# Kernel optimization log

Measured on AMD Instinct MI355X. Metric: run time of the kernel, lower is better.

Reference implementation:

```python
import jax, jax.numpy as jnp
import numpy as np

NU, NI, NE, NR = 100000, 50000, 200000, 64
D, K, EDGES, L, B = 64, 16, 2000000, 2, 4096
REG = 1e-4


def setup_inputs() -> dict:
    key = jax.random.key(0)
    ks = jax.random.split(key, 18)
    f = lambda k, sh: jax.random.normal(k, sh, dtype=jnp.float32)
    return {
        # embedding tables (init std=0.01 as in the torch module)
        'user_emb_w': f(ks[0], (NU, D)) * 0.01,
        'item_emb_w': f(ks[1], (NI, D)) * 0.01,
        'entity_emb_w': f(ks[2], (NE, D)) * 0.01,
        'relation_emb_w': f(ks[3], (NR, D)) * 0.01,
        # per-layer linear params (stacked over L layers)
        'Wk_w': f(ks[4], (L, D, 2 * D)) * 0.05,
        'Wk_b': f(ks[5], (L, D)) * 0.05,
        'Wa_w': f(ks[6], (L, D, D)) * 0.05,
        'Wa_b': f(ks[7], (L, D)) * 0.05,
        'Wb_w': f(ks[8], (L, D, D)) * 0.05,
        'Wb_b': f(ks[9], (L, D)) * 0.05,
        'edge_norm': jax.random.uniform(ks[10], (EDGES,), dtype=jnp.float32),
        # BPR batch ids
        'user': jax.random.randint(ks[11], (B,), 0, NU, dtype=jnp.int32),
        'pos_item': jax.random.randint(ks[12], (B,), 0, NI, dtype=jnp.int32),
        'neg_item': jax.random.randint(ks[13], (B,), 0, NI, dtype=jnp.int32),
        # interaction graph edge lists
        'edge_u': jax.random.randint(ks[14], (EDGES,), 0, NU, dtype=jnp.int32),
        'edge_i': jax.random.randint(ks[15], (EDGES,), 0, NI, dtype=jnp.int32),
        # KG neighbors: K (relation, entity) pairs per item
        'kg_rel': jax.random.randint(ks[16], (NI, K), 0, NR, dtype=jnp.int32),
        'kg_ent': jax.random.randint(ks[17], (NI, K), 0, NE, dtype=jnp.int32),
    }


def reference(user_emb_w, item_emb_w, entity_emb_w, relation_emb_w,
              Wk_w, Wk_b, Wa_w, Wa_b, Wb_w, Wb_b, edge_norm,
              user, pos_item, neg_item, edge_u, edge_i, kg_rel, kg_ent):
    # KG neighbor gathers (entity/relation tables are constant across layers)
    v = entity_emb_w[kg_ent]        # [NI, K, D]
    r = relation_emb_w[kg_rel]      # [NI, K, D]
    norm = edge_norm[:, None]       # [E, 1]

    u_cur, i_cur = user_emb_w, item_emb_w
    u_sum, i_sum = user_emb_w, item_emb_w
    for l in range(L):
        # --- KG attention (vectorized over all items and neighbors) ---
        hv = v * i_cur[:, None, :]                            # [NI, K, D]
        # concat([hv, hv]) @ Wk.T == hv @ (Wk[:, :D] + Wk[:, D:]).T
        w_eff = Wk_w[l][:, :D] + Wk_w[l][:, D:]               # [D, D]
        proj = jnp.einsum('ikd,od->iko', hv, w_eff) + Wk_b[l]  # [NI, K, D]
        score = jax.nn.leaky_relu(jnp.sum(r * proj, axis=-1), 0.2)  # [NI, K]
        alpha = jax.nn.softmax(score, axis=-1)                # softmax over neighbors
        kg_item = jnp.einsum('ik,ikd->id', alpha, v)          # [NI, D]
        # --- LightGCN propagation (segment scatter-add) ---
        agg_i = jax.ops.segment_sum(norm * u_cur[edge_u], edge_i, num_segments=NI)
        agg_u = jax.ops.segment_sum(norm * i_cur[edge_i], edge_u, num_segments=NU)
        # --- Gated fusion ---
        gate = jax.nn.sigmoid(kg_item @ Wa_w[l].T + Wa_b[l]
                              + agg_i @ Wb_w[l].T + Wb_b[l])
        i_cur = gate * kg_item + (1.0 - gate) * agg_i
        u_cur = agg_u
        u_sum = u_sum + u_cur
        i_sum = i_sum + i_cur

    # --- BPR loss ---
    u_e = u_sum[user]
    pos_e = i_sum[pos_item]
    neg_e = i_sum[neg_item]
    pos_s = jnp.sum(u_e * pos_e, axis=-1)
    neg_s = jnp.sum(u_e * neg_e, axis=-1)
    bpr = -jnp.mean(jnp.log(jax.nn.sigmoid(pos_s - neg_s) + 1e-10))
    l2 = (jnp.sum(u_e ** 2) + jnp.sum(pos_e ** 2) + jnp.sum(neg_e ** 2)) / user.shape[0]
    return bpr + REG * l2
```

## Files before the change

kernel.cpp:

```cpp
#include <hip/hip_runtime.h>
#include <math.h>

constexpr int DD    = 64;
constexpr int KK    = 16;
constexpr int NUs   = 100000;
constexpr int NIs   = 50000;
constexpr int NEs   = 200000;
constexpr int NRs   = 64;
constexpr int NEDGE = 2000000;
constexpr int LAYERS = 2;
constexpr int BB    = 4096;
constexpr float REGf = 1e-4f;

constexpr int SUBB  = 256;
constexpr int NB_I  = (NIs + SUBB - 1) / SUBB;
constexpr int NB_U  = (NUs + SUBB - 1) / SUBB;
constexpr int NBT   = NB_I + NB_U;
constexpr int CH    = 8192;
constexpr int NCHK  = (NEDGE + CH - 1) / CH;

__device__ __forceinline__ float wave_sum_f(float x) {
#pragma unroll
  for (int off = 32; off > 0; off >>= 1) x += __shfl_xor(x, off);
  return x;
}


__global__ __launch_bounds__(256) void bhist_kernel(const int* __restrict__ edge_u,
                                                    const int* __restrict__ edge_i,
                                                    int* __restrict__ gbkt) {
  __shared__ int lcnt[NBT];
  for (int b = threadIdx.x; b < NBT; b += 256) lcnt[b] = 0;
  __syncthreads();
  int base = blockIdx.x * CH;
  for (int k = threadIdx.x; k < CH; k += 256) {
    int e = base + k;
    if (e < NEDGE) {
      atomicAdd(&lcnt[edge_i[e] >> 8], 1);
      atomicAdd(&lcnt[NB_I + (edge_u[e] >> 8)], 1);
    }
  }
  __syncthreads();
  for (int b = threadIdx.x; b < NBT; b += 256) {
    int c = lcnt[b];
    if (c) atomicAdd(&gbkt[b], c);
  }
}

__global__ __launch_bounds__(1024) void bscan_kernel(const int* __restrict__ gbkt,
                                                     int* __restrict__ bktbase,
                                                     int* __restrict__ bktcur,
                                                     int* rp_i, int* rp_u) {
  __shared__ int sv[1024];
  int tid = threadIdx.x;
  int x = (tid < NBT) ? gbkt[tid] : 0;
  bool segU = (tid >= NB_I);
  int v = x;
  sv[tid] = v;
  __syncthreads();
  for (int off = 1; off < 1024; off <<= 1) {
    int y = 0;
    if (tid >= off) {
      int o = tid - off;
      if ((o >= NB_I) == segU) y = sv[o];
    }
    __syncthreads();
    v += y;
    sv[tid] = v;
    __syncthreads();
  }
  if (tid < NBT) {
    int ex = v - x;
    bktbase[tid] = ex;
    bktcur[tid] = ex;
  }
  if (tid == 0) { rp_i[NIs] = NEDGE; rp_u[NUs] = NEDGE; }
}

__global__ __launch_bounds__(256) void bscatter_kernel(const int* __restrict__ edge_u,
                                                       const int* __restrict__ edge_i,
                                                       const float* __restrict__ enorm,
                                                       int* __restrict__ bktcur,
                                                       int2* __restrict__ tmp_i,
                                                       int2* __restrict__ tmp_u) {
  __shared__ int lcnt[NBT];
  __shared__ int lbase[NBT];
  for (int b = threadIdx.x; b < NBT; b += 256) lcnt[b] = 0;
  __syncthreads();
  int base = blockIdx.x * CH;
  for (int k = threadIdx.x; k < CH; k += 256) {
    int e = base + k;
    if (e < NEDGE) {
      atomicAdd(&lcnt[edge_i[e] >> 8], 1);
      atomicAdd(&lcnt[NB_I + (edge_u[e] >> 8)], 1);
    }
  }
  __syncthreads();
  for (int b = threadIdx.x; b < NBT; b += 256) {
    int c = lcnt[b];
    lbase[b] = c ? atomicAdd(&bktcur[b], c) : 0;
    lcnt[b] = 0;
  }
  __syncthreads();
  for (int k = threadIdx.x; k < CH; k += 256) {
    int e = base + k;
    if (e < NEDGE) {
      int it = edge_i[e], u = edge_u[e];
      int wb = __float_as_int(enorm[e]);
      int bi = it >> 8;
      int p = lbase[bi] + atomicAdd(&lcnt[bi], 1);
      tmp_i[p] = make_int2(((it & 255) << 20) | u, wb);
      int bu = NB_I + (u >> 8);
      int q = lbase[bu] + atomicAdd(&lcnt[bu], 1);
      tmp_u[q] = make_int2(((u & 255) << 20) | it, wb);
    }
  }
}

__global__ __launch_bounds__(256) void bsort_kernel(const int* __restrict__ gbkt,
                                                    const int* __restrict__ bktbase,
                                                    const int2* __restrict__ tmp_i,
                                                    const int2* __restrict__ tmp_u,
                                                    int2* __restrict__ pair_i,
                                                    int2* __restrict__ pair_u,
                                                    int* __restrict__ rp_i,
                                                    int* __restrict__ rp_u) {
  int b = blockIdx.x;
  bool isI = (b < NB_I);
  const int2* tmp = isI ? tmp_i : tmp_u;
  int2* po = isI ? pair_i : pair_u;
  int* rp = isI ? rp_i : rp_u;
  int ndst = isI ? NIs : NUs;
  int localb = isI ? b : b - NB_I;
  int start = bktbase[b];
  int size = gbkt[b];
  __shared__ int dcnt[256];
  __shared__ int dpos[256];
  __shared__ int wt[4];
  int tid = threadIdx.x;
  dcnt[tid] = 0;
  __syncthreads();
  for (int k = tid; k < size; k += 256) atomicAdd(&dcnt[tmp[start + k].x >> 20], 1);
  __syncthreads();
  int c = dcnt[tid];
  int lane = tid & 63, wid = tid >> 6;
  int v = c;
#pragma unroll
  for (int off = 1; off < 64; off <<= 1) {
    int y = __shfl_up(v, off);
    if (lane >= off) v += y;
  }
  if (lane == 63) wt[wid] = v;
  __syncthreads();
  int woff = 0;
#pragma unroll
  for (int w = 0; w < 4; ++w)
    if (w < wid) woff += wt[w];
  int excl = woff + v - c;
  dpos[tid] = excl;
  int idx = localb * 256 + tid;
  if (idx < ndst) rp[idx] = start + excl;
  dcnt[tid] = 0;
  __syncthreads();
  for (int k = tid; k < size; k += 256) {
    int2 pw = tmp[start + k];
    int sub = pw.x >> 20;
    int j = dpos[sub] + atomicAdd(&dcnt[sub], 1);
    po[start + j] = make_int2(pw.x & 0xFFFFF, pw.y);
  }
}

__global__ __launch_bounds__(64) void rt_kernel(const float* __restrict__ RE,
                                                const float* __restrict__ Wkw,
                                                const float* __restrict__ Wkb,
                                                float* Rt, float* cvec) {
  int l = blockIdx.x >> 6;
  int n = blockIdx.x & 63;
  int d = threadIdx.x;
  const float* W  = Wkw + (size_t)l * DD * 2 * DD;
  const float* re = RE + n * DD;
  float acc = 0.f;
  for (int o = 0; o < DD; ++o) {
    float w = W[o * 2 * DD + d] + W[o * 2 * DD + DD + d];
    acc += re[o] * w;
  }
  Rt[(l * NRs + n) * DD + d] = acc;
  float p = re[d] * Wkb[l * DD + d];
  p = wave_sum_f(p);
  if (d == 0) cvec[l * NRs + n] = p;
}

__global__ __launch_bounds__(256) void attn_kernel(const float* __restrict__ EE,
                                                   const float* __restrict__ Rt_l,
                                                   const float* __restrict__ c_l,
                                                   const int* __restrict__ kg_ent,
                                                   const int* __restrict__ kg_rel,
                                                   const float* __restrict__ i_cur,
                                                   float* __restrict__ kg_item) {
  int tid = threadIdx.x;
  int l16 = tid & 15;
  int gbase = ((tid & 63) >> 4) << 4;
  int gid = blockIdx.x * 16 + (tid >> 4);
  int ngrp = gridDim.x * 16;
  for (int i = gid; i < NIs; i += ngrp) {
    float4 ic = reinterpret_cast<const float4*>(i_cur + ((size_t)i << 6))[l16];
    int ent = kg_ent[i * KK + l16];
    int rel = kg_rel[i * KK + l16];
    float4 vk[KK];
#pragma unroll
    for (int k = 0; k < KK; ++k) {
      int e = __shfl(ent, gbase + k);
      vk[k] = reinterpret_cast<const float4*>(EE + ((size_t)e << 6))[l16];
    }
    float sc[KK];
#pragma unroll
    for (int k = 0; k < KK; ++k) {
      int rl = __shfl(rel, gbase + k);
      float4 rt = reinterpret_cast<const float4*>(Rt_l + ((size_t)rl << 6))[l16];
      float p = vk[k].x * ic.x * rt.x + vk[k].y * ic.y * rt.y
              + vk[k].z * ic.z * rt.z + vk[k].w * ic.w * rt.w;
      p += __shfl_xor(p, 1); p += __shfl_xor(p, 2);
      p += __shfl_xor(p, 4); p += __shfl_xor(p, 8);
      float s = p + c_l[rl];
      sc[k] = (s >= 0.f) ? s : 0.2f * s;
    }
    float m = sc[0];
#pragma unroll
    for (int k = 1; k < KK; ++k) m = fmaxf(m, sc[k]);
    float ssum = 0.f;
#pragma unroll
    for (int k = 0; k < KK; ++k) { sc[k] = __expf(sc[k] - m); ssum += sc[k]; }
    float inv = 1.f / ssum;
    float4 o = make_float4(0.f, 0.f, 0.f, 0.f);
#pragma unroll
    for (int k = 0; k < KK; ++k) {
      float a = sc[k] * inv;
      o.x += a * vk[k].x; o.y += a * vk[k].y;
      o.z += a * vk[k].z; o.w += a * vk[k].w;
    }
    reinterpret_cast<float4*>(kg_item + ((size_t)i << 6))[l16] = o;
  }
}

__global__ __launch_bounds__(256) void agg2_kernel(
    const int* __restrict__ rp_i, const int2* __restrict__ pair_i,
    const float* __restrict__ embU, float* __restrict__ aggi,
    const int* __restrict__ rp_u, const int2* __restrict__ pair_u,
    const float* __restrict__ embI, float* __restrict__ unext,
    float* __restrict__ usum, const float* __restrict__ usum_init) {
  int tid = threadIdx.x;
  int l16 = tid & 15;
  int gbase = ((tid & 63) >> 4) << 4;
  int gid = blockIdx.x * 16 + (tid >> 4);
  int ngrp = gridDim.x * 16;
  const int total = NIs + NUs;
  for (int row = gid; row < total; row += ngrp) {
    bool isU = row >= NIs;
    int r = isU ? (row - NIs) : row;
    const int*  rp = isU ? rp_u   : rp_i;
    const int2* pr = isU ? pair_u : pair_i;
    const float* emb = isU ? embI : embU;
    int s0 = rp[r], s1 = rp[r + 1];
    float4 accA = make_float4(0.f, 0.f, 0.f, 0.f);
    float4 accB = make_float4(0.f, 0.f, 0.f, 0.f);
    for (int base = s0; base < s1; base += 16) {
      int lim = s1 - base;
      int sj = 0; float wj = 0.f;
      if (l16 < lim) {
        int2 pw = pr[base + l16];
        sj = pw.x; wj = __int_as_float(pw.y);
      }
#pragma unroll
      for (int jj = 0; jj < 8; ++jj) {
        int aA = __shfl(sj, gbase + jj);     float qA = __shfl(wj, gbase + jj);
        int aB = __shfl(sj, gbase + 8 + jj); float qB = __shfl(wj, gbase + 8 + jj);
        float4 eA = reinterpret_cast<const float4*>(emb + ((size_t)aA << 6))[l16];
        float4 eB = reinterpret_cast<const float4*>(emb + ((size_t)aB << 6))[l16];
        accA.x += qA * eA.x; accA.y += qA * eA.y; accA.z += qA * eA.z; accA.w += qA * eA.w;
        accB.x += qB * eB.x; accB.y += qB * eB.y; accB.z += qB * eB.z; accB.w += qB * eB.w;
      }
    }
    float4 o;
    o.x = accA.x + accB.x; o.y = accA.y + accB.y;
    o.z = accA.z + accB.z; o.w = accA.w + accB.w;
    if (!isU) {
      reinterpret_cast<float4*>(aggi + ((size_t)r << 6))[l16] = o;
    } else {
      reinterpret_cast<float4*>(unext + ((size_t)r << 6))[l16] = o;
      float4 si;
      if (usum_init) si = reinterpret_cast<const float4*>(usum_init + ((size_t)r << 6))[l16];
      else           si = reinterpret_cast<float4*>(usum + ((size_t)r << 6))[l16];
      float4 s;
      s.x = si.x + o.x; s.y = si.y + o.y; s.z = si.z + o.z; s.w = si.w + o.w;
      reinterpret_cast<float4*>(usum + ((size_t)r << 6))[l16] = s;
    }
  }
}

__global__ __launch_bounds__(256) void gate_kernel(const float* __restrict__ Wa,
                                                   const float* __restrict__ Wab,
                                                   const float* __restrict__ Wb,
                                                   const float* __restrict__ Wbb,
                                                   const float* __restrict__ kg_item,
                                                   const float* __restrict__ agg_i,
                                                   const float* __restrict__ i_sum_init,
                                                   float* __restrict__ i_next,
                                                   float* __restrict__ i_sum) {
  __shared__ float at[DD * 65];
  __shared__ float bt[DD * 65];
  for (int m = threadIdx.x; m < DD * DD; m += blockDim.x) {
    int o = m >> 6, d = m & 63;
    at[d * 65 + o] = Wa[m];
    bt[d * 65 + o] = Wb[m];
  }
  __syncthreads();
  int lane = threadIdx.x & 63, wid = threadIdx.x >> 6;
  int wpg = gridDim.x * (blockDim.x >> 6);
  float wab = Wab[lane], wbb = Wbb[lane];
  for (int i = blockIdx.x * (blockDim.x >> 6) + wid; i < NIs; i += wpg) {
    float kg = kg_item[i * DD + lane];
    float ag = agg_i[i * DD + lane];
    float acca = 0.f, accb = 0.f;
#pragma unroll
    for (int d = 0; d < DD; ++d) {
      float kd = __shfl(kg, d);
      float ad = __shfl(ag, d);
      acca += kd * at[d * 65 + lane];
      accb += ad * bt[d * 65 + lane];
    }
    float g = 1.f / (1.f + __expf(-(acca + wab + accb + wbb)));
    float inew = g * kg + (1.f - g) * ag;
    i_next[i * DD + lane] = inew;
    if (i_sum_init) i_sum[i * DD + lane] = i_sum_init[i * DD + lane] + inew;
    else            i_sum[i * DD + lane] += inew;
  }
}

__global__ __launch_bounds__(256) void loss_kernel(const float* __restrict__ u_sum,
                                                   const float* __restrict__ i_sum,
                                                   const int* __restrict__ user,
                                                   const int* __restrict__ pos,
                                                   const int* __restrict__ neg,
                                                   float* acc) {
  int lane = threadIdx.x & 63, wid = threadIdx.x >> 6;
  int wpg = gridDim.x * (blockDim.x >> 6);
  float lacc = 0.f, l2acc = 0.f;
  for (int b = blockIdx.x * (blockDim.x >> 6) + wid; b < BB; b += wpg) {
    float u = u_sum[user[b] * DD + lane];
    float p = i_sum[pos[b] * DD + lane];
    float n = i_sum[neg[b] * DD + lane];
    float ps = wave_sum_f(u * p);
    float ns = wave_sum_f(u * n);
    float sq = wave_sum_f(u * u + p * p + n * n);
    if (lane == 0) {
      float x = ps - ns;
      float sig = 1.f / (1.f + expf(-x));
      lacc += logf(sig + 1e-10f);
      l2acc += sq;
    }
  }
  if (lane == 0) {
    atomicAdd(&acc[0], lacc);
    atomicAdd(&acc[1], l2acc);
  }
}

__global__ void final_kernel(const float* acc, float* out) {
  out[0] = -acc[0] / (float)BB + REGf * (acc[1] / (float)BB);
}


extern "C" void kernel_launch(void* const* d_in, const int* in_sizes, int n_in,
                              void* d_out, int out_size, void* d_ws, size_t ws_size,
                              hipStream_t stream) {
  const float* UE   = (const float*)d_in[0];
  const float* IE   = (const float*)d_in[1];
  const float* EE   = (const float*)d_in[2];
  const float* RE   = (const float*)d_in[3];
  const float* Wkw  = (const float*)d_in[4];
  const float* Wkb  = (const float*)d_in[5];
  const float* Waw  = (const float*)d_in[6];
  const float* Wab  = (const float*)d_in[7];
  const float* Wbw  = (const float*)d_in[8];
  const float* Wbb  = (const float*)d_in[9];
  const float* enorm = (const float*)d_in[10];
  const int* user   = (const int*)d_in[11];
  const int* pos    = (const int*)d_in[12];
  const int* neg    = (const int*)d_in[13];
  const int* edge_u = (const int*)d_in[14];
  const int* edge_i = (const int*)d_in[15];
  const int* kg_rel = (const int*)d_in[16];
  const int* kg_ent = (const int*)d_in[17];

  size_t off = 0;
  char* base = (char*)d_ws;
  auto take = [&](size_t bytes) -> void* {
    void* p = base + off;
    off += (bytes + 255) & ~(size_t)255;
    return p;
  };
  float* Rt      = (float*)take(LAYERS * NRs * DD * sizeof(float));
  float* cvec    = (float*)take(LAYERS * NRs * sizeof(float));
  float* acc     = (float*)take(8 * sizeof(float));
  int*   gbkt    = (int*)take(NBT * sizeof(int));
  int*   bktbase = (int*)take(NBT * sizeof(int));
  int*   bktcur  = (int*)take(NBT * sizeof(int));
  int*   rp_i    = (int*)take((NIs + 1) * sizeof(int));
  int*   rp_u    = (int*)take((NUs + 1) * sizeof(int));
  int2*  tmp_i   = (int2*)take((size_t)NEDGE * sizeof(int2));
  int2*  tmp_u   = (int2*)take((size_t)NEDGE * sizeof(int2));
  int2*  pair_i  = (int2*)take((size_t)NEDGE * sizeof(int2));
  int2*  pair_u  = (int2*)take((size_t)NEDGE * sizeof(int2));
  float* kg      = (float*)take((size_t)NIs * DD * sizeof(float));
  float* aggi    = (float*)take((size_t)NIs * DD * sizeof(float));
  float* iA      = (float*)take((size_t)NIs * DD * sizeof(float));
  float* iB      = (float*)take((size_t)NIs * DD * sizeof(float));
  float* isum    = (float*)take((size_t)NIs * DD * sizeof(float));
  float* uA      = (float*)take((size_t)NUs * DD * sizeof(float));
  float* uB      = (float*)take((size_t)NUs * DD * sizeof(float));
  float* usum    = (float*)take((size_t)NUs * DD * sizeof(float));
  (void)ws_size; (void)in_sizes; (void)n_in; (void)out_size;

  hipMemsetAsync(gbkt, 0, NBT * sizeof(int), stream);
  hipMemsetAsync(acc, 0, 8 * sizeof(float), stream);

  bhist_kernel<<<NCHK, 256, 0, stream>>>(edge_u, edge_i, gbkt);
  bscan_kernel<<<1, 1024, 0, stream>>>(gbkt, bktbase, bktcur, rp_i, rp_u);
  bscatter_kernel<<<NCHK, 256, 0, stream>>>(edge_u, edge_i, enorm, bktcur, tmp_i, tmp_u);
  bsort_kernel<<<NBT, 256, 0, stream>>>(gbkt, bktbase, tmp_i, tmp_u,
                                        pair_i, pair_u, rp_i, rp_u);
  rt_kernel<<<LAYERS * NRs, 64, 0, stream>>>(RE, Wkw, Wkb, Rt, cvec);

  const float* u_cur = UE;
  const float* i_cur = IE;
  float* unext[2] = {uA, uB};
  float* inext[2] = {iA, iB};
  for (int l = 0; l < LAYERS; ++l) {
    attn_kernel<<<2048, 256, 0, stream>>>(EE, Rt + l * NRs * DD, cvec + l * NRs,
                                          kg_ent, kg_rel, i_cur, kg);
    agg2_kernel<<<2048, 256, 0, stream>>>(rp_i, pair_i, u_cur, aggi,
                                          rp_u, pair_u, i_cur, unext[l],
                                          usum, (l == 0) ? UE : nullptr);
    gate_kernel<<<2048, 256, 0, stream>>>(Waw + (size_t)l * DD * DD, Wab + l * DD,
                                          Wbw + (size_t)l * DD * DD, Wbb + l * DD,
                                          kg, aggi, (l == 0) ? IE : nullptr,
                                          inext[l], isum);
    u_cur = unext[l];
    i_cur = inext[l];
  }

  loss_kernel<<<1024, 256, 0, stream>>>(usum, isum, user, pos, neg, acc);
  final_kernel<<<1, 1, 0, stream>>>(acc, (float*)d_out);
}
```

Baseline: 941.1 us.

## Fuse attention, aggregation and gating into one per-layer kernel; merge small launches

Merges the KG attention, LightGCN aggregation and gated fusion kernels into a single layer kernel. The kg_item and agg_i intermediates now stay in registers instead of going through global memory. The rt computation is folded into the scan kernel's extra blocks, the memsets become one prep kernel, and the final kernel is replaced by a last-block-done reduction inside the loss kernel, which also drops from 1024 to 256 blocks. In exchange, item rows and user rows now run different code paths inside one kernel, which can cause imbalance, and every block must load the transposed gate weights into shared memory.

```diff
diff --git a/kernel.cpp b/kernel.cpp
--- a/kernel.cpp
+++ b/kernel.cpp
@@ -25,6 +25,12 @@
   return x;
 }
 
+__global__ __launch_bounds__(256) void prep_kernel(int* gbkt, float* acc, int* done) {
+  for (int b = threadIdx.x; b < NBT; b += 256) gbkt[b] = 0;
+  if (threadIdx.x < 8) acc[threadIdx.x] = 0.f;
+  if (threadIdx.x == 8) *done = 0;
+}
+
 
 __global__ __launch_bounds__(256) void bhist_kernel(const int* __restrict__ edge_u,
                                                     const int* __restrict__ edge_i,
@@ -47,34 +53,55 @@
   }
 }
 
-__global__ __launch_bounds__(1024) void bscan_kernel(const int* __restrict__ gbkt,
-                                                     int* __restrict__ bktbase,
-                                                     int* __restrict__ bktcur,
-                                                     int* rp_i, int* rp_u) {
-  __shared__ int sv[1024];
-  int tid = threadIdx.x;
-  int x = (tid < NBT) ? gbkt[tid] : 0;
-  bool segU = (tid >= NB_I);
-  int v = x;
-  sv[tid] = v;
-  __syncthreads();
-  for (int off = 1; off < 1024; off <<= 1) {
-    int y = 0;
-    if (tid >= off) {
-      int o = tid - off;
-      if ((o >= NB_I) == segU) y = sv[o];
-    }
-    __syncthreads();
-    v += y;
+__global__ __launch_bounds__(1024) void bscan_rt_kernel(const int* __restrict__ gbkt,
+                                                        int* __restrict__ bktbase,
+                                                        int* __restrict__ bktcur,
+                                                        int* rp_i, int* rp_u,
+                                                        const float* __restrict__ RE,
+                                                        const float* __restrict__ Wkw,
+                                                        const float* __restrict__ Wkb,
+                                                        float* Rt, float* cvec) {
+  if (blockIdx.x == 0) {
+    __shared__ int sv[1024];
+    int tid = threadIdx.x;
+    int x = (tid < NBT) ? gbkt[tid] : 0;
+    bool segU = (tid >= NB_I);
+    int v = x;
     sv[tid] = v;
     __syncthreads();
-  }
-  if (tid < NBT) {
-    int ex = v - x;
-    bktbase[tid] = ex;
-    bktcur[tid] = ex;
-  }
-  if (tid == 0) { rp_i[NIs] = NEDGE; rp_u[NUs] = NEDGE; }
+    for (int off = 1; off < 1024; off <<= 1) {
+      int y = 0;
+      if (tid >= off) {
+        int o = tid - off;
+        if ((o >= NB_I) == segU) y = sv[o];
+      }
+      __syncthreads();
+      v += y;
+      sv[tid] = v;
+      __syncthreads();
+    }
+    if (tid < NBT) {
+      int ex = v - x;
+      bktbase[tid] = ex;
+      bktcur[tid] = ex;
+    }
+    if (tid == 0) { rp_i[NIs] = NEDGE; rp_u[NUs] = NEDGE; }
+  } else {
+    int p = (blockIdx.x - 1) * 16 + (threadIdx.x >> 6);
+    int l = p >> 6, n = p & 63;
+    int d = threadIdx.x & 63;
+    const float* W  = Wkw + (size_t)l * DD * 2 * DD;
+    const float* re = RE + n * DD;
+    float acc = 0.f;
+    for (int o = 0; o < DD; ++o) {
+      float w = W[o * 2 * DD + d] + W[o * 2 * DD + DD + d];
+      acc += re[o] * w;
+    }
+    Rt[(l * NRs + n) * DD + d] = acc;
+    float pr = re[d] * Wkb[l * DD + d];
+    pr = wave_sum_f(pr);
+    if (d == 0) cvec[l * NRs + n] = pr;
+  }
 }
 
 __global__ __launch_bounds__(256) void bscatter_kernel(const int* __restrict__ edge_u,
@@ -170,84 +197,27 @@
   }
 }
 
-__global__ __launch_bounds__(64) void rt_kernel(const float* __restrict__ RE,
-                                                const float* __restrict__ Wkw,
-                                                const float* __restrict__ Wkb,
-                                                float* Rt, float* cvec) {
-  int l = blockIdx.x >> 6;
-  int n = blockIdx.x & 63;
-  int d = threadIdx.x;
-  const float* W  = Wkw + (size_t)l * DD * 2 * DD;
-  const float* re = RE + n * DD;
-  float acc = 0.f;
-  for (int o = 0; o < DD; ++o) {
-    float w = W[o * 2 * DD + d] + W[o * 2 * DD + DD + d];
-    acc += re[o] * w;
-  }
-  Rt[(l * NRs + n) * DD + d] = acc;
-  float p = re[d] * Wkb[l * DD + d];
-  p = wave_sum_f(p);
-  if (d == 0) cvec[l * NRs + n] = p;
-}
-
-__global__ __launch_bounds__(256) void attn_kernel(const float* __restrict__ EE,
-                                                   const float* __restrict__ Rt_l,
-                                                   const float* __restrict__ c_l,
-                                                   const int* __restrict__ kg_ent,
-                                                   const int* __restrict__ kg_rel,
-                                                   const float* __restrict__ i_cur,
-                                                   float* __restrict__ kg_item) {
-  int tid = threadIdx.x;
-  int l16 = tid & 15;
-  int gbase = ((tid & 63) >> 4) << 4;
-  int gid = blockIdx.x * 16 + (tid >> 4);
-  int ngrp = gridDim.x * 16;
-  for (int i = gid; i < NIs; i += ngrp) {
-    float4 ic = reinterpret_cast<const float4*>(i_cur + ((size_t)i << 6))[l16];
-    int ent = kg_ent[i * KK + l16];
-    int rel = kg_rel[i * KK + l16];
-    float4 vk[KK];
-#pragma unroll
-    for (int k = 0; k < KK; ++k) {
-      int e = __shfl(ent, gbase + k);
-      vk[k] = reinterpret_cast<const float4*>(EE + ((size_t)e << 6))[l16];
-    }
-    float sc[KK];
-#pragma unroll
-    for (int k = 0; k < KK; ++k) {
-      int rl = __shfl(rel, gbase + k);
-      float4 rt = reinterpret_cast<const float4*>(Rt_l + ((size_t)rl << 6))[l16];
-      float p = vk[k].x * ic.x * rt.x + vk[k].y * ic.y * rt.y
-              + vk[k].z * ic.z * rt.z + vk[k].w * ic.w * rt.w;
-      p += __shfl_xor(p, 1); p += __shfl_xor(p, 2);
-      p += __shfl_xor(p, 4); p += __shfl_xor(p, 8);
-      float s = p + c_l[rl];
-      sc[k] = (s >= 0.f) ? s : 0.2f * s;
-    }
-    float m = sc[0];
-#pragma unroll
-    for (int k = 1; k < KK; ++k) m = fmaxf(m, sc[k]);
-    float ssum = 0.f;
-#pragma unroll
-    for (int k = 0; k < KK; ++k) { sc[k] = __expf(sc[k] - m); ssum += sc[k]; }
-    float inv = 1.f / ssum;
-    float4 o = make_float4(0.f, 0.f, 0.f, 0.f);
-#pragma unroll
-    for (int k = 0; k < KK; ++k) {
-      float a = sc[k] * inv;
-      o.x += a * vk[k].x; o.y += a * vk[k].y;
-      o.z += a * vk[k].z; o.w += a * vk[k].w;
-    }
-    reinterpret_cast<float4*>(kg_item + ((size_t)i << 6))[l16] = o;
-  }
-}
-
-__global__ __launch_bounds__(256) void agg2_kernel(
+__global__ __launch_bounds__(256) void layer_kernel(
+    const float* __restrict__ EE, const float* __restrict__ Rt_l,
+    const float* __restrict__ c_l,
+    const int* __restrict__ kg_ent, const int* __restrict__ kg_rel,
+    const float* __restrict__ Waw_l, const float* __restrict__ Wab_l,
+    const float* __restrict__ Wbw_l, const float* __restrict__ Wbb_l,
     const int* __restrict__ rp_i, const int2* __restrict__ pair_i,
-    const float* __restrict__ embU, float* __restrict__ aggi,
     const int* __restrict__ rp_u, const int2* __restrict__ pair_u,
-    const float* __restrict__ embI, float* __restrict__ unext,
-    float* __restrict__ usum, const float* __restrict__ usum_init) {
+    const float* __restrict__ u_cur, const float* __restrict__ i_cur,
+    float* __restrict__ i_next, float* __restrict__ i_sum,
+    const float* __restrict__ i_sum_init,
+    float* __restrict__ u_next, float* __restrict__ u_sum,
+    const float* __restrict__ u_sum_init) {
+  __shared__ float at_s[DD * DD];
+  __shared__ float bt_s[DD * DD];
+  for (int m = threadIdx.x; m < DD * DD; m += 256) {
+    int o = m >> 6, d = m & 63;
+    at_s[d * 64 + o] = Waw_l[m];
+    bt_s[d * 64 + o] = Wbw_l[m];
+  }
+  __syncthreads();
   int tid = threadIdx.x;
   int l16 = tid & 15;
   int gbase = ((tid & 63) >> 4) << 4;
@@ -255,84 +225,143 @@
   int ngrp = gridDim.x * 16;
   const int total = NIs + NUs;
   for (int row = gid; row < total; row += ngrp) {
-    bool isU = row >= NIs;
-    int r = isU ? (row - NIs) : row;
-    const int*  rp = isU ? rp_u   : rp_i;
-    const int2* pr = isU ? pair_u : pair_i;
-    const float* emb = isU ? embI : embU;
-    int s0 = rp[r], s1 = rp[r + 1];
-    float4 accA = make_float4(0.f, 0.f, 0.f, 0.f);
-    float4 accB = make_float4(0.f, 0.f, 0.f, 0.f);
-    for (int base = s0; base < s1; base += 16) {
-      int lim = s1 - base;
-      int sj = 0; float wj = 0.f;
-      if (l16 < lim) {
-        int2 pw = pr[base + l16];
-        sj = pw.x; wj = __int_as_float(pw.y);
-      }
-#pragma unroll
-      for (int jj = 0; jj < 8; ++jj) {
-        int aA = __shfl(sj, gbase + jj);     float qA = __shfl(wj, gbase + jj);
-        int aB = __shfl(sj, gbase + 8 + jj); float qB = __shfl(wj, gbase + 8 + jj);
-        float4 eA = reinterpret_cast<const float4*>(emb + ((size_t)aA << 6))[l16];
-        float4 eB = reinterpret_cast<const float4*>(emb + ((size_t)aB << 6))[l16];
-        accA.x += qA * eA.x; accA.y += qA * eA.y; accA.z += qA * eA.z; accA.w += qA * eA.w;
-        accB.x += qB * eB.x; accB.y += qB * eB.y; accB.z += qB * eB.z; accB.w += qB * eB.w;
-      }
-    }
-    float4 o;
-    o.x = accA.x + accB.x; o.y = accA.y + accB.y;
-    o.z = accA.z + accB.z; o.w = accA.w + accB.w;
-    if (!isU) {
-      reinterpret_cast<float4*>(aggi + ((size_t)r << 6))[l16] = o;
+    if (row < NIs) {
+      int i = row;
+      float4 ic = reinterpret_cast<const float4*>(i_cur + ((size_t)i << 6))[l16];
+      int ent = kg_ent[i * KK + l16];
+      int rel = kg_rel[i * KK + l16];
+      float4 vk[KK];
+#pragma unroll
+      for (int k = 0; k < KK; ++k) {
+        int e = __shfl(ent, gbase + k);
+        vk[k] = reinterpret_cast<const float4*>(EE + ((size_t)e << 6))[l16];
+      }
+      float sc[KK];
+#pragma unroll
+      for (int k = 0; k < KK; ++k) {
+        int rl = __shfl(rel, gbase + k);
+        float4 rt = reinterpret_cast<const float4*>(Rt_l + ((size_t)rl << 6))[l16];
+        float p = vk[k].x * ic.x * rt.x + vk[k].y * ic.y * rt.y
+                + vk[k].z * ic.z * rt.z + vk[k].w * ic.w * rt.w;
+        p += __shfl_xor(p, 1); p += __shfl_xor(p, 2);
+        p += __shfl_xor(p, 4); p += __shfl_xor(p, 8);
+        float s = p + c_l[rl];
+        sc[k] = (s >= 0.f) ? s : 0.2f * s;
+      }
+      float mx = sc[0];
+#pragma unroll
+      for (int k = 1; k < KK; ++k) mx = fmaxf(mx, sc[k]);
+      float ssum = 0.f;
+#pragma unroll
+      for (int k = 0; k < KK; ++k) { sc[k] = __expf(sc[k] - mx); ssum += sc[k]; }
+      float inv = 1.f / ssum;
+      float4 kg = make_float4(0.f, 0.f, 0.f, 0.f);
+#pragma unroll
+      for (int k = 0; k < KK; ++k) {
+        float a = sc[k] * inv;
+        kg.x += a * vk[k].x; kg.y += a * vk[k].y;
+        kg.z += a * vk[k].z; kg.w += a * vk[k].w;
+      }
+      int s0 = rp_i[i], s1 = rp_i[i + 1];
+      float4 accA = make_float4(0.f, 0.f, 0.f, 0.f);
+      float4 accB = make_float4(0.f, 0.f, 0.f, 0.f);
+      for (int base = s0; base < s1; base += 16) {
+        int lim = s1 - base;
+        int sj = 0; float wj = 0.f;
+        if (l16 < lim) {
+          int2 pw = pair_i[base + l16];
+          sj = pw.x; wj = __int_as_float(pw.y);
+        }
+#pragma unroll
+        for (int jj = 0; jj < 8; ++jj) {
+          int aA = __shfl(sj, gbase + jj);     float qA = __shfl(wj, gbase + jj);
+          int aB = __shfl(sj, gbase + 8 + jj); float qB = __shfl(wj, gbase + 8 + jj);
+          float4 eA = reinterpret_cast<const float4*>(u_cur + ((size_t)aA << 6))[l16];
+          float4 eB = reinterpret_cast<const float4*>(u_cur + ((size_t)aB << 6))[l16];
+          accA.x += qA * eA.x; accA.y += qA * eA.y; accA.z += qA * eA.z; accA.w += qA * eA.w;
+          accB.x += qB * eB.x; accB.y += qB * eB.y; accB.z += qB * eB.z; accB.w += qB * eB.w;
+        }
+      }
+      float4 ag;
+      ag.x = accA.x + accB.x; ag.y = accA.y + accB.y;
+      ag.z = accA.z + accB.z; ag.w = accA.w + accB.w;
+      float4 acca = make_float4(0.f, 0.f, 0.f, 0.f);
+      float4 accb = make_float4(0.f, 0.f, 0.f, 0.f);
+#pragma unroll
+      for (int r = 0; r < 16; ++r) {
+        float kx = __shfl(kg.x, gbase + r), ky = __shfl(kg.y, gbase + r);
+        float kz = __shfl(kg.z, gbase + r), kw = __shfl(kg.w, gbase + r);
+        float axv = __shfl(ag.x, gbase + r), ayv = __shfl(ag.y, gbase + r);
+        float azv = __shfl(ag.z, gbase + r), awv = __shfl(ag.w, gbase + r);
+        float4 a0 = *reinterpret_cast<const float4*>(&at_s[(4 * r + 0) * 64 + l16 * 4]);
+        float4 a1 = *reinterpret_cast<const float4*>(&at_s[(4 * r + 1) * 64 + l16 * 4]);
+        float4 a2 = *reinterpret_cast<const float4*>(&at_s[(4 * r + 2) * 64 + l16 * 4]);
+        float4 a3 = *reinterpret_cast<const float4*>(&at_s[(4 * r + 3) * 64 + l16 * 4]);
+        acca.x += kx * a0.x + ky * a1.x + kz * a2.x + kw * a3.x;
+        acca.y += kx * a0.y + ky * a1.y + kz * a2.y + kw * a3.y;
+        acca.z += kx * a0.z + ky * a1.z + kz * a2.z + kw * a3.z;
+        acca.w += kx * a0.w + ky * a1.w + kz * a2.w + kw * a3.w;
+        float4 b0 = *reinterpret_cast<const float4*>(&bt_s[(4 * r + 0) * 64 + l16 * 4]);
+        float4 b1 = *reinterpret_cast<const float4*>(&bt_s[(4 * r + 1) * 64 + l16 * 4]);
+        float4 b2 = *reinterpret_cast<const float4*>(&bt_s[(4 * r + 2) * 64 + l16 * 4]);
+        float4 b3 = *reinterpret_cast<const float4*>(&bt_s[(4 * r + 3) * 64 + l16 * 4]);
+        accb.x += axv * b0.x + ayv * b1.x + azv * b2.x + awv * b3.x;
+        accb.y += axv * b0.y + ayv * b1.y + azv * b2.y + awv * b3.y;
+        accb.z += axv * b0.z + ayv * b1.z + azv * b2.z + awv * b3.z;
+        accb.w += axv * b0.w + ayv * b1.w + azv * b2.w + awv * b3.w;
+      }
+      float4 wab = reinterpret_cast<const float4*>(Wab_l)[l16];
+      float4 wbb = reinterpret_cast<const float4*>(Wbb_l)[l16];
+      float4 g, inew;
+      g.x = 1.f / (1.f + __expf(-(acca.x + wab.x + accb.x + wbb.x)));
+      g.y = 1.f / (1.f + __expf(-(acca.y + wab.y + accb.y + wbb.y)));
+      g.z = 1.f / (1.f + __expf(-(acca.z + wab.z + accb.z + wbb.z)));
+      g.w = 1.f / (1.f + __expf(-(acca.w + wab.w + accb.w + wbb.w)));
+      inew.x = g.x * kg.x + (1.f - g.x) * ag.x;
+      inew.y = g.y * kg.y + (1.f - g.y) * ag.y;
+      inew.z = g.z * kg.z + (1.f - g.z) * ag.z;
+      inew.w = g.w * kg.w + (1.f - g.w) * ag.w;
+      reinterpret_cast<float4*>(i_next + ((size_t)i << 6))[l16] = inew;
+      float4 si;
+      if (i_sum_init) si = reinterpret_cast<const float4*>(i_sum_init + ((size_t)i << 6))[l16];
+      else            si = reinterpret_cast<float4*>(i_sum + ((size_t)i << 6))[l16];
+      float4 so;
+      so.x = si.x + inew.x; so.y = si.y + inew.y;
+      so.z = si.z + inew.z; so.w = si.w + inew.w;
+      reinterpret_cast<float4*>(i_sum + ((size_t)i << 6))[l16] = so;
     } else {
-      reinterpret_cast<float4*>(unext + ((size_t)r << 6))[l16] = o;
+      int r = row - NIs;
+      int s0 = rp_u[r], s1 = rp_u[r + 1];
+      float4 accA = make_float4(0.f, 0.f, 0.f, 0.f);
+      float4 accB = make_float4(0.f, 0.f, 0.f, 0.f);
+      for (int base = s0; base < s1; base += 16) {
+        int lim = s1 - base;
+        int sj = 0; float wj = 0.f;
+        if (l16 < lim) {
+          int2 pw = pair_u[base + l16];
+          sj = pw.x; wj = __int_as_float(pw.y);
+        }
+#pragma unroll
+        for (int jj = 0; jj < 8; ++jj) {
+          int aA = __shfl(sj, gbase + jj);     float qA = __shfl(wj, gbase + jj);
+          int aB = __shfl(sj, gbase + 8 + jj); float qB = __shfl(wj, gbase + 8 + jj);
+          float4 eA = reinterpret_cast<const float4*>(i_cur + ((size_t)aA << 6))[l16];
+          float4 eB = reinterpret_cast<const float4*>(i_cur + ((size_t)aB << 6))[l16];
+          accA.x += qA * eA.x; accA.y += qA * eA.y; accA.z += qA * eA.z; accA.w += qA * eA.w;
+          accB.x += qB * eB.x; accB.y += qB * eB.y; accB.z += qB * eB.z; accB.w += qB * eB.w;
+        }
+      }
+      float4 o;
+      o.x = accA.x + accB.x; o.y = accA.y + accB.y;
+      o.z = accA.z + accB.z; o.w = accA.w + accB.w;
+      reinterpret_cast<float4*>(u_next + ((size_t)r << 6))[l16] = o;
       float4 si;
-      if (usum_init) si = reinterpret_cast<const float4*>(usum_init + ((size_t)r << 6))[l16];
-      else           si = reinterpret_cast<float4*>(usum + ((size_t)r << 6))[l16];
+      if (u_sum_init) si = reinterpret_cast<const float4*>(u_sum_init + ((size_t)r << 6))[l16];
+      else            si = reinterpret_cast<float4*>(u_sum + ((size_t)r << 6))[l16];
       float4 s;
       s.x = si.x + o.x; s.y = si.y + o.y; s.z = si.z + o.z; s.w = si.w + o.w;
-      reinterpret_cast<float4*>(usum + ((size_t)r << 6))[l16] = s;
-    }
-  }
-}
-
-__global__ __launch_bounds__(256) void gate_kernel(const float* __restrict__ Wa,
-                                                   const float* __restrict__ Wab,
-                                                   const float* __restrict__ Wb,
-                                                   const float* __restrict__ Wbb,
-                                                   const float* __restrict__ kg_item,
-                                                   const float* __restrict__ agg_i,
-                                                   const float* __restrict__ i_sum_init,
-                                                   float* __restrict__ i_next,
-                                                   float* __restrict__ i_sum) {
-  __shared__ float at[DD * 65];
-  __shared__ float bt[DD * 65];
-  for (int m = threadIdx.x; m < DD * DD; m += blockDim.x) {
-    int o = m >> 6, d = m & 63;
-    at[d * 65 + o] = Wa[m];
-    bt[d * 65 + o] = Wb[m];
-  }
-  __syncthreads();
-  int lane = threadIdx.x & 63, wid = threadIdx.x >> 6;
-  int wpg = gridDim.x * (blockDim.x >> 6);
-  float wab = Wab[lane], wbb = Wbb[lane];
-  for (int i = blockIdx.x * (blockDim.x >> 6) + wid; i < NIs; i += wpg) {
-    float kg = kg_item[i * DD + lane];
-    float ag = agg_i[i * DD + lane];
-    float acca = 0.f, accb = 0.f;
-#pragma unroll
-    for (int d = 0; d < DD; ++d) {
-      float kd = __shfl(kg, d);
-      float ad = __shfl(ag, d);
-      acca += kd * at[d * 65 + lane];
-      accb += ad * bt[d * 65 + lane];
-    }
-    float g = 1.f / (1.f + __expf(-(acca + wab + accb + wbb)));
-    float inew = g * kg + (1.f - g) * ag;
-    i_next[i * DD + lane] = inew;
-    if (i_sum_init) i_sum[i * DD + lane] = i_sum_init[i * DD + lane] + inew;
-    else            i_sum[i * DD + lane] += inew;
+      reinterpret_cast<float4*>(u_sum + ((size_t)r << 6))[l16] = s;
+    }
   }
 }
 
@@ -341,7 +370,7 @@
                                                    const int* __restrict__ user,
                                                    const int* __restrict__ pos,
                                                    const int* __restrict__ neg,
-                                                   float* acc) {
+                                                   float* acc, int* done, float* out) {
   int lane = threadIdx.x & 63, wid = threadIdx.x >> 6;
   int wpg = gridDim.x * (blockDim.x >> 6);
   float lacc = 0.f, l2acc = 0.f;
@@ -363,10 +392,16 @@
     atomicAdd(&acc[0], lacc);
     atomicAdd(&acc[1], l2acc);
   }
-}
-
-__global__ void final_kernel(const float* acc, float* out) {
-  out[0] = -acc[0] / (float)BB + REGf * (acc[1] / (float)BB);
+  __syncthreads();
+  if (threadIdx.x == 0) {
+    __threadfence();
+    int old = atomicAdd(done, 1);
+    if (old == gridDim.x - 1) {
+      float a0 = atomicAdd(&acc[0], 0.f);
+      float a1 = atomicAdd(&acc[1], 0.f);
+      out[0] = -a0 / (float)BB + REGf * (a1 / (float)BB);
+    }
+  }
 }
 
 
@@ -402,6 +437,7 @@
   float* Rt      = (float*)take(LAYERS * NRs * DD * sizeof(float));
   float* cvec    = (float*)take(LAYERS * NRs * sizeof(float));
   float* acc     = (float*)take(8 * sizeof(float));
+  int*   done    = (int*)take(sizeof(int));
   int*   gbkt    = (int*)take(NBT * sizeof(int));
   int*   bktbase = (int*)take(NBT * sizeof(int));
   int*   bktcur  = (int*)take(NBT * sizeof(int));
@@ -411,8 +447,6 @@
   int2*  tmp_u   = (int2*)take((size_t)NEDGE * sizeof(int2));
   int2*  pair_i  = (int2*)take((size_t)NEDGE * sizeof(int2));
   int2*  pair_u  = (int2*)take((size_t)NEDGE * sizeof(int2));
-  float* kg      = (float*)take((size_t)NIs * DD * sizeof(float));
-  float* aggi    = (float*)take((size_t)NIs * DD * sizeof(float));
   float* iA      = (float*)take((size_t)NIs * DD * sizeof(float));
   float* iB      = (float*)take((size_t)NIs * DD * sizeof(float));
   float* isum    = (float*)take((size_t)NIs * DD * sizeof(float));
@@ -421,34 +455,29 @@
   float* usum    = (float*)take((size_t)NUs * DD * sizeof(float));
   (void)ws_size; (void)in_sizes; (void)n_in; (void)out_size;
 
-  hipMemsetAsync(gbkt, 0, NBT * sizeof(int), stream);
-  hipMemsetAsync(acc, 0, 8 * sizeof(float), stream);
-
+  prep_kernel<<<1, 256, 0, stream>>>(gbkt, acc, done);
   bhist_kernel<<<NCHK, 256, 0, stream>>>(edge_u, edge_i, gbkt);
-  bscan_kernel<<<1, 1024, 0, stream>>>(gbkt, bktbase, bktcur, rp_i, rp_u);
+  bscan_rt_kernel<<<9, 1024, 0, stream>>>(gbkt, bktbase, bktcur, rp_i, rp_u,
+                                          RE, Wkw, Wkb, Rt, cvec);
   bscatter_kernel<<<NCHK, 256, 0, stream>>>(edge_u, edge_i, enorm, bktcur, tmp_i, tmp_u);
   bsort_kernel<<<NBT, 256, 0, stream>>>(gbkt, bktbase, tmp_i, tmp_u,
                                         pair_i, pair_u, rp_i, rp_u);
-  rt_kernel<<<LAYERS * NRs, 64, 0, stream>>>(RE, Wkw, Wkb, Rt, cvec);
 
   const float* u_cur = UE;
   const float* i_cur = IE;
   float* unext[2] = {uA, uB};
   float* inext[2] = {iA, iB};
   for (int l = 0; l < LAYERS; ++l) {
-    attn_kernel<<<2048, 256, 0, stream>>>(EE, Rt + l * NRs * DD, cvec + l * NRs,
-                                          kg_ent, kg_rel, i_cur, kg);
-    agg2_kernel<<<2048, 256, 0, stream>>>(rp_i, pair_i, u_cur, aggi,
-                                          rp_u, pair_u, i_cur, unext[l],
-                                          usum, (l == 0) ? UE : nullptr);
-    gate_kernel<<<2048, 256, 0, stream>>>(Waw + (size_t)l * DD * DD, Wab + l * DD,
-                                          Wbw + (size_t)l * DD * DD, Wbb + l * DD,
-                                          kg, aggi, (l == 0) ? IE : nullptr,
-                                          inext[l], isum);
+    layer_kernel<<<2048, 256, 0, stream>>>(
+        EE, Rt + l * NRs * DD, cvec + l * NRs, kg_ent, kg_rel,
+        Waw + (size_t)l * DD * DD, Wab + l * DD,
+        Wbw + (size_t)l * DD * DD, Wbb + l * DD,
+        rp_i, pair_i, rp_u, pair_u, u_cur, i_cur,
+        inext[l], isum, (l == 0) ? IE : nullptr,
+        unext[l], usum, (l == 0) ? UE : nullptr);
     u_cur = unext[l];
     i_cur = inext[l];
   }
 
-  loss_kernel<<<1024, 256, 0, stream>>>(usum, isum, user, pos, neg, acc);
-  final_kernel<<<1, 1, 0, stream>>>(acc, (float*)d_out);
-}
+  loss_kernel<<<256, 256, 0, stream>>>(usum, isum, user, pos, neg, acc, done, (float*)d_out);
+}
```

New measurement: 835.8 us. 1.13x faster.
